# Optimization experiments

Hardware: AMD Instinct MI355X
Metric: run time of the kernel (lower is better)

## Reference

```python
import jax, jax.numpy as jnp
import numpy as np

EPS = 1e-8
LN_EPS = 1e-5
NEG = -1e9
H, E, D, P = 4, 32, 8, 64          # heads, embed_dim, head_dim, particles (= input_dim)
N_LAYERS, N_CLS = 4, 2
N_BATCH = 2048
F_EXTRA = 60                        # x feature channels; F_EXTRA + 4 == P == input_dim


def _ln(x):
    m = jnp.mean(x, -1, keepdims=True)
    v = jnp.mean((x - m) ** 2, -1, keepdims=True)
    return (x - m) * jax.lax.rsqrt(v + LN_EPS)


def _lin(x, w, b):
    return x @ w.T + b


def _gelu(x):
    return jax.nn.gelu(x, approximate=False)


def _mha(q_in, kv, in_w, in_b, out_w, out_b, attn_bias, kpm):
    # torch nn.MultiheadAttention, batch_first=False. q_in: (L,N,E), kv: (S,N,E)
    L, N, _ = q_in.shape
    S = kv.shape[0]
    q = _lin(q_in, in_w[:E], in_b[:E]) * (D ** -0.5)
    k = _lin(kv, in_w[E:2 * E], in_b[E:2 * E])
    v = _lin(kv, in_w[2 * E:], in_b[2 * E:])
    q = q.reshape(L, N, H, D); k = k.reshape(S, N, H, D); v = v.reshape(S, N, H, D)
    s = jnp.einsum('lnhd,snhd->nhls', q, k)
    if attn_bias is not None:
        s = s + attn_bias.reshape(N, H, L, S)
    s = jnp.where(kpm[:, None, None, :], NEG, s)
    a = jax.nn.softmax(s, -1)
    o = jnp.einsum('nhls,snhd->lnhd', a, v).reshape(L, N, E)
    return _lin(o, out_w, out_b)


def _jet_features(v):
    # vectorized calculate_jet_features_; v: (N,4,P). All pair features are symmetric,
    # diagonal stays zero (python loop skipped i==j), features are detached.
    e, px, py, pz = v[:, 0], v[:, 1], v[:, 2], v[:, 3]
    pt = jnp.sqrt(px ** 2 + py ** 2 + EPS)
    y = 0.5 * jnp.log((e + pz + EPS) / (e - pz + EPS))
    phi = jnp.mod(jnp.arctan2(py, px + EPS), 2.0 * np.pi)   # already in [0, 2pi)
    r = lambda a: a[:, :, None]
    c = lambda a: a[:, None, :]
    dist = (r(px) + c(px)) ** 2 + (r(py) + c(py)) ** 2 + (r(pz) + c(pz)) ** 2
    delta = jnp.sqrt(jnp.abs((r(y) - c(y)) ** 2 + (r(phi) - c(phi)) ** 2))
    pmin = jnp.minimum(r(pt), c(pt))
    kt = pmin * delta
    z = pmin / (r(pt) + c(pt) + EPS)
    m2 = r(e) ** 2 + c(e) ** 2 - dist
    f = jnp.stack([delta, kt, z, m2], axis=1)               # (N,4,P,P)
    f = f * (1.0 - jnp.eye(v.shape[2], dtype=f.dtype))
    return jax.lax.stop_gradient(f)


def _conv2d(x, w, b, stride, pad):
    y = jax.lax.conv_general_dilated(x, w, (stride, stride), [(pad, pad), (pad, pad)],
                                     dimension_numbers=('NCHW', 'OIHW', 'NCHW'))
    return y + b[None, :, None, None]


def _forward(x, four_momenta, jet_inputs, bn_w, bn_b, e1_w, e1_b, e2_w, e2_b,
             c1_w, c1_b, c2_w, c2_b,
             pb_in_w, pb_in_b, pb_out_w, pb_out_b, pb_f1_w, pb_f1_b, pb_f2_w, pb_f2_b, pb_wres,
             cb_in_w, cb_in_b, cb_out_w, cb_out_b, cb_f1_w, cb_f1_b, cb_f2_w, cb_f2_b, cb_wres,
             cb_cattn, cls_token, norm_w, norm_b, m1_w, m1_b, mh_w, mh_b, mf_w, mf_b):
    N = x.shape[0]
    xc = jnp.concatenate([x, four_momenta], axis=1)                 # (N, P, P): channels == particles
    kpm = ~(jnp.arange(P)[None, :] < jet_inputs[:, 1][:, None])     # (N, P) True = padded key
    xb = jnp.transpose(xc, (0, 2, 1))                               # (N, C=P, L=input_dim)
    mu = jnp.mean(xb, axis=(0, 2), keepdims=True)
    var = jnp.var(xb, axis=(0, 2), keepdims=True)
    xb = (xb - mu) * jax.lax.rsqrt(var + LN_EPS) * bn_w[None, :, None] + bn_b[None, :, None]
    h = jnp.transpose(xb, (2, 0, 1))                                # (seq, N, P)
    h = _gelu(_lin(_ln(h), e1_w, e1_b))
    h = _gelu(_lin(_ln(h), e2_w, e2_b))                             # (P, N, E)
    # --- PairEmbed: pairwise kinematic features -> 2 convs -> per-head attention bias
    f = _jet_features(four_momenta)                                 # (N, 4, P, P)
    cpe = _conv2d(f, c1_w, c1_b, 4, 0)                              # (N, H, 16, 16)
    cpe = _conv2d(cpe, c2_w, c2_b, 2, 1)                            # (N, H, 9, 9)
    bias = cpe.reshape(N * H, 9, 9)
    bias = jnp.pad(bias, ((0, 0), (0, P - 9), (0, P - 9)))          # additive bias zero-padded to (N*H,P,P)
    # --- particle blocks
    for i in range(N_LAYERS):
        res = h
        a = _ln(h)
        a = _mha(a, a, pb_in_w[i], pb_in_b[i], pb_out_w[i], pb_out_b[i], bias, kpm)
        h = _ln(a) + res
        res = h
        g = _gelu(_lin(_ln(h), pb_f1_w[i], pb_f1_b[i]))
        g = _lin(_ln(g), pb_f2_w[i], pb_f2_b[i])
        h = g + pb_wres[i] * res
    # --- class-attention blocks
    kpm_cls = jnp.concatenate([jnp.zeros((N, 1), dtype=bool), kpm], axis=1)
    cls = jnp.broadcast_to(cls_token, (1, N, E))
    for i in range(N_CLS):
        res = cls
        u = _ln(jnp.concatenate([cls, h], axis=0))                  # pre_attn_norm on keys/values only
        a = _mha(cls, u, cb_in_w[i], cb_in_b[i], cb_out_w[i], cb_out_b[i], None, kpm_cls)
        # tbhd,h->tbdh then reshape flattens as (d, h) order, matching torch
        a = jnp.einsum('tbhd,h->tbdh', a.reshape(1, N, H, D), cb_cattn[i]).reshape(1, N, E)
        cls = _ln(a) + res
        res = cls
        g = _gelu(_lin(_ln(cls), cb_f1_w[i], cb_f1_b[i]))
        g = _lin(_ln(g), cb_f2_w[i], cb_f2_b[i])
        cls = g + cb_wres[i] * res
    # --- head: affine LayerNorm + MLP (the two transposes in MLP cancel)
    z = (_ln(cls) * norm_w + norm_b)[0]                             # (N, E)
    z = jax.nn.relu(_lin(z, m1_w, m1_b))
    z = jax.nn.relu(_lin(z, mh_w, mh_b))
    z = jax.nn.sigmoid(_lin(z, mf_w, mf_b))                         # (N, 1)
    return z.reshape(-1)


def setup_inputs():
    key = jax.random.key(0)
    ks = jax.random.split(key, 40)
    w = lambda k, s: (0.05 * jax.random.normal(k, s)).astype(jnp.float32)
    p3 = jax.random.normal(ks[0], (N_BATCH, 3, P), dtype=jnp.float32)
    en = jnp.sqrt(jnp.sum(p3 ** 2, axis=1, keepdims=True) + 0.1)    # physical: E > |pz|
    four_momenta = jnp.concatenate([en, p3], axis=1)
    return {
        'x': jax.random.normal(ks[1], (N_BATCH, F_EXTRA, P), dtype=jnp.float32),
        'four_momenta': four_momenta,
        'jet_inputs': jax.random.randint(ks[2], (N_BATCH, 2), 1, P + 1),
        'bn_w': jnp.ones((P,), jnp.float32), 'bn_b': jnp.zeros((P,), jnp.float32),
        'e1_w': w(ks[3], (64, P)), 'e1_b': w(ks[4], (64,)),
        'e2_w': w(ks[5], (E, 64)), 'e2_b': w(ks[6], (E,)),
        'c1_w': w(ks[7], (H, 4, 4, 4)), 'c1_b': w(ks[8], (H,)),
        'c2_w': w(ks[9], (H, H, 2, 2)), 'c2_b': w(ks[10], (H,)),
        'pb_in_w': w(ks[11], (N_LAYERS, 3 * E, E)), 'pb_in_b': w(ks[12], (N_LAYERS, 3 * E)),
        'pb_out_w': w(ks[13], (N_LAYERS, E, E)), 'pb_out_b': w(ks[14], (N_LAYERS, E)),
        'pb_f1_w': w(ks[15], (N_LAYERS, 2 * E, E)), 'pb_f1_b': w(ks[16], (N_LAYERS, 2 * E)),
        'pb_f2_w': w(ks[17], (N_LAYERS, E, 2 * E)), 'pb_f2_b': w(ks[18], (N_LAYERS, E)),
        'pb_wres': jnp.ones((N_LAYERS, E), jnp.float32),
        'cb_in_w': w(ks[19], (N_CLS, 3 * E, E)), 'cb_in_b': w(ks[20], (N_CLS, 3 * E)),
        'cb_out_w': w(ks[21], (N_CLS, E, E)), 'cb_out_b': w(ks[22], (N_CLS, E)),
        'cb_f1_w': w(ks[23], (N_CLS, 2 * E, E)), 'cb_f1_b': w(ks[24], (N_CLS, 2 * E)),
        'cb_f2_w': w(ks[25], (N_CLS, E, 2 * E)), 'cb_f2_b': w(ks[26], (N_CLS, E)),
        'cb_wres': jnp.ones((N_CLS, E), jnp.float32),
        'cb_cattn': jnp.ones((N_CLS, H), jnp.float32),
        'cls_token': w(ks[27], (1, 1, E)),
        'norm_w': jnp.ones((E,), jnp.float32), 'norm_b': jnp.zeros((E,), jnp.float32),
        'm1_w': w(ks[28], (32, E)), 'm1_b': w(ks[29], (32,)),
        'mh_w': w(ks[30], (32, 32)), 'mh_b': w(ks[31], (32,)),
        'mf_w': w(ks[32], (1, 32)), 'mf_b': w(ks[33], (1,)),
    }


def reference(x, four_momenta, jet_inputs, bn_w, bn_b, e1_w, e1_b, e2_w, e2_b,
              c1_w, c1_b, c2_w, c2_b,
              pb_in_w, pb_in_b, pb_out_w, pb_out_b, pb_f1_w, pb_f1_b, pb_f2_w, pb_f2_b, pb_wres,
              cb_in_w, cb_in_b, cb_out_w, cb_out_b, cb_f1_w, cb_f1_b, cb_f2_w, cb_f2_b, cb_wres,
              cb_cattn, cls_token, norm_w, norm_b, m1_w, m1_b, mh_w, mh_b, mf_w, mf_b):
    return _forward(x, four_momenta, jet_inputs, bn_w, bn_b, e1_w, e1_b, e2_w, e2_b,
                    c1_w, c1_b, c2_w, c2_b,
                    pb_in_w, pb_in_b, pb_out_w, pb_out_b, pb_f1_w, pb_f1_b, pb_f2_w, pb_f2_b, pb_wres,
                    cb_in_w, cb_in_b, cb_out_w, cb_out_b, cb_f1_w, cb_f1_b, cb_f2_w, cb_f2_b, cb_wres,
                    cb_cattn, cls_token, norm_w, norm_b, m1_w, m1_b, mh_w, mh_b, mf_w, mf_b)
```

## Files before the change

kernel.cpp:

```cpp
#include <hip/hip_runtime.h>


__device__ __forceinline__ float4 ld4(const float* p){ return *reinterpret_cast<const float4*>(p); }
__device__ __forceinline__ float dot4(float4 a, float4 b){ return a.x*b.x + a.y*b.y + a.z*b.z + a.w*b.w; }
__device__ __forceinline__ float geluf(float v){ return 0.5f*v*(1.0f + erff(v*0.70710678118654752f)); }

__global__ void bn_stats_partial(const float* __restrict__ x, const float* __restrict__ fm,
                                 float* __restrict__ part) {
  int p  = threadIdx.x & 63;
  int rg = threadIdx.x >> 6;
  float s = 0.f, s2 = 0.f;
  for (int R = blockIdx.x*4 + rg; R < 2048*64; R += 1024) {
    int n_ = R >> 6, c = R & 63;
    float v = (c < 60) ? x[n_*3840 + c*64 + p] : fm[n_*256 + (c-60)*64 + p];
    s += v; s2 += v*v;
  }
  __shared__ float sm[256], sm2[256];
  sm[threadIdx.x] = s; sm2[threadIdx.x] = s2;
  __syncthreads();
  if (threadIdx.x < 64) {
    part[blockIdx.x*128 + p]      = sm[p]+sm[64+p]+sm[128+p]+sm[192+p];
    part[blockIdx.x*128 + 64 + p] = sm2[p]+sm2[64+p]+sm2[128+p]+sm2[192+p];
  }
}

__global__ void bn_stats_final(const float* __restrict__ part, float* __restrict__ stats) {
  int p = threadIdx.x;
  float s = 0.f, s2 = 0.f;
  for (int b = 0; b < 256; b++){ s += part[b*128+p]; s2 += part[b*128+64+p]; }
  float mean = s * (1.f/131072.f);
  float var  = s2 * (1.f/131072.f) - mean*mean;
  stats[p]      = mean;
  stats[64+p]   = rsqrtf(var + 1e-5f);
}

__device__ __forceinline__ void ln_rows32(const float* src, float* dst, int tid){
  int r = tid>>2, g = tid&3;
  const float* row = src + r*36;
  float v[8]; float s = 0.f;
  #pragma unroll
  for (int k=0;k<8;k++){ v[k] = row[g*8+k]; s += v[k]; }
  s += __shfl_xor(s,1); s += __shfl_xor(s,2);
  float mean = s * 0.03125f;
  float q = 0.f;
  #pragma unroll
  for (int k=0;k<8;k++){ float d = v[k]-mean; q += d*d; }
  q += __shfl_xor(q,1); q += __shfl_xor(q,2);
  float irs = rsqrtf(q*0.03125f + 1e-5f);
  float* drow = dst + r*36;
  #pragma unroll
  for (int k=0;k<8;k++) drow[g*8+k] = (v[k]-mean)*irs;
}

__device__ __forceinline__ void ln_rows64(const float* src, float* dst, int tid){
  int r = tid>>2, g = tid&3;
  const float* row = src + r*68;
  float v[16]; float s = 0.f;
  #pragma unroll
  for (int k=0;k<16;k++){ v[k] = row[g*16+k]; s += v[k]; }
  s += __shfl_xor(s,1); s += __shfl_xor(s,2);
  float mean = s * 0.015625f;
  float q = 0.f;
  #pragma unroll
  for (int k=0;k<16;k++){ float d = v[k]-mean; q += d*d; }
  q += __shfl_xor(q,1); q += __shfl_xor(q,2);
  float irs = rsqrtf(q*0.015625f + 1e-5f);
  float* drow = dst + r*68;
  #pragma unroll
  for (int k=0;k<16;k++) drow[g*16+k] = (v[k]-mean)*irs;
}

__global__ __launch_bounds__(256) void k_feat(
    const float* __restrict__ fm,
    const float* __restrict__ c1w_g, const float* __restrict__ c1b_g,
    const float* __restrict__ c2w_g, const float* __restrict__ c2b_g,
    float* __restrict__ G_bias)
{
  const int n   = blockIdx.x;
  const int tid = threadIdx.x;
  __shared__ float PQ[448];
  __shared__ float C1O[1024];
  __shared__ float CW[328];

  if (tid < 64) {
    int p = tid;
    float e_  = fm[n*256 + p];
    float px_ = fm[n*256 + 64 + p];
    float py_ = fm[n*256 + 128 + p];
    float pz_ = fm[n*256 + 192 + p];
    float pt_ = sqrtf(px_*px_ + py_*py_ + 1e-8f);
    float y_  = 0.5f * logf((e_ + pz_ + 1e-8f) / (e_ - pz_ + 1e-8f));
    float ph_ = atan2f(py_, px_ + 1e-8f);
    if (ph_ < 0.f) ph_ += 6.283185307179586f;
    PQ[0*64+p]=e_; PQ[1*64+p]=px_; PQ[2*64+p]=py_; PQ[3*64+p]=pz_;
    PQ[4*64+p]=pt_; PQ[5*64+p]=y_; PQ[6*64+p]=ph_;
  }
  CW[tid < 256 ? tid : 0] = c1w_g[tid < 256 ? tid : 0];
  if (tid < 4)  CW[256+tid] = c1b_g[tid];
  if (tid < 64) CW[260+tid] = c2w_g[tid];
  if (tid < 4)  CW[324+tid] = c2b_g[tid];
  __syncthreads();

  {
    int ho = tid>>4, wo = tid&15;
    float a0=0.f,a1=0.f,a2=0.f,a3=0.f;
    #pragma unroll 1
    for (int kh=0; kh<4; kh++){
      int r = ho*4+kh;
      float er=PQ[r], pxr=PQ[64+r], pyr=PQ[128+r], pzr=PQ[192+r], ptr_=PQ[256+r], yr=PQ[320+r], phr=PQ[384+r];
      #pragma unroll
      for (int kw=0; kw<4; kw++){
        int c = wo*4+kw;
        if (r == c) continue;
        float ec=PQ[c], pxc=PQ[64+c], pyc=PQ[128+c], pzc=PQ[192+c], ptc=PQ[256+c], yc=PQ[320+c], phc=PQ[384+c];
        float dy = yr-yc, dp = phr-phc;
        float delta = sqrtf(fabsf(dy*dy + dp*dp));
        float pmin = fminf(ptr_, ptc);
        float kt = pmin * delta;
        float zz = pmin / (ptr_ + ptc + 1e-8f);
        float sx_ = pxr+pxc, sy_ = pyr+pyc, sz_ = pzr+pzc;
        float m2 = er*er + ec*ec - (sx_*sx_ + sy_*sy_ + sz_*sz_);
        int wb = kh*4+kw;
// ... 78 lines not shown
      #pragma unroll
      for (int i=0;i<4;i++) acc[i][o] = b; }
    #pragma unroll 2
    for (int j=0;j<64;j+=4){
      float4 av[4], wv[4];
      #pragma unroll
      for (int i=0;i<4;i++) av[i] = ld4(SY + (tg*4+i)*68 + j);
      #pragma unroll
      for (int o=0;o<4;o++) wv[o] = ld4(SW + (og*4+o)*68 + j);
      #pragma unroll
      for (int i=0;i<4;i++)
        #pragma unroll
        for (int o=0;o<4;o++) acc[i][o] += dot4(av[i], wv[o]);
    }
    __syncthreads();
    #pragma unroll
    for (int i=0;i<4;i++)
      #pragma unroll
      for (int o=0;o<4;o++) SX[(tg*4+i)*68 + og*4+o] = geluf(acc[i][o]);
  }
  __syncthreads();

  ln_rows64(SX, SY, tid);
  for (int idx = tid; idx < 2048; idx += 256){ SW[(idx>>6)*68 + (idx&63)] = e2w[idx]; }
  for (int idx = tid; idx < 32; idx += 256) SW[4352+idx] = e2b[idx];
  __syncthreads();

  {
    int tg = tid>>4, og = tid&15;
    float acc[4][2];
    #pragma unroll
    for (int o=0;o<2;o++){ float b = SW[4352+og*2+o];
      #pragma unroll
      for (int i=0;i<4;i++) acc[i][o] = b; }
    #pragma unroll 2
    for (int j=0;j<64;j+=4){
      float4 av[4], wv[2];
      #pragma unroll
      for (int i=0;i<4;i++) av[i] = ld4(SY + (tg*4+i)*68 + j);
      #pragma unroll
      for (int o=0;o<2;o++) wv[o] = ld4(SW + (og*2+o)*68 + j);
      #pragma unroll
      for (int i=0;i<4;i++)
        #pragma unroll
        for (int o=0;o<2;o++) acc[i][o] += dot4(av[i], wv[o]);
    }
    #pragma unroll
    for (int i=0;i<4;i++)
      #pragma unroll
      for (int o=0;o<2;o++) G_h[n*2048 + (tg*4+i)*32 + og*2+o] = geluf(acc[i][o]);
  }
}

__global__ __launch_bounds__(256, 3) void k_layer(
    const int* __restrict__ ji,
    const float* __restrict__ in_w,  const float* __restrict__ in_b,
    const float* __restrict__ out_w, const float* __restrict__ out_b,
    const float* __restrict__ f1w,   const float* __restrict__ f1b,
    const float* __restrict__ f2w,   const float* __restrict__ f2b,
    const float* __restrict__ wres,
    float* __restrict__ G_h, const float* __restrict__ G_bias)
{
  const int n   = blockIdx.x;
  const int tid = threadIdx.x;

  __shared__ __align__(16) float SH[64*36];
  __shared__ __align__(16) float SX[64*36];
  __shared__ __align__(16) float SY[64*68];
  __shared__ __align__(16) float SW[3584];
  __shared__ float SBIAS[324];
  __shared__ int s_njet;

  if (tid == 0) s_njet = ji[n*2+1];
  for (int idx = tid; idx < 2048; idx += 256) {
    int t = idx>>5, e = idx&31;
    SH[t*36 + e] = G_h[n*2048 + idx];
  }
  for (int idx = tid; idx < 324; idx += 256) SBIAS[idx] = G_bias[n*324 + idx];
  __syncthreads();

  ln_rows32(SH, SX, tid);
  for (int idx = tid; idx < 3072; idx += 256){ SW[(idx>>5)*36 + (idx&31)] = in_w[idx]; }
  for (int idx = tid; idx < 96; idx += 256) SW[3456+idx] = in_b[idx];
  __syncthreads();

  {
    int tg = tid>>4, og = tid&15;
    float acc[4][4];
    #pragma unroll
    for (int o=0;o<4;o++){ float b = SW[3456+32+og*4+o];
      #pragma unroll
      for (int i=0;i<4;i++) acc[i][o] = b; }
    #pragma unroll 2
    for (int j=0;j<32;j+=4){
      float4 av[4], wv[4];
      #pragma unroll
      for (int i=0;i<4;i++) av[i] = ld4(SX + (tg*4+i)*36 + j);
      #pragma unroll
      for (int o=0;o<4;o++) wv[o] = ld4(SW + (32+og*4+o)*36 + j);
      #pragma unroll
      for (int i=0;i<4;i++)
        #pragma unroll
        for (int o=0;o<4;o++) acc[i][o] += dot4(av[i], wv[o]);
    }
    #pragma unroll
    for (int i=0;i<4;i++)
      #pragma unroll
      for (int o=0;o<4;o++){
        int ew = 32 + og*4+o, t = tg*4+i;
        if (ew < 64) SY[(ew-32)*68 + t] = acc[i][o];
        else         SY[2176 + (ew-64)*68 + t] = acc[i][o];
      }
  }
  __syncthreads();

  float od[8];
  {
    int hh = tid>>6, l = tid&63;
    float qd[8];
    #pragma unroll
    for (int d=0;d<8;d++){
      int e = hh*8+d;
      float a_ = SW[3456+e];
      #pragma unroll
      for (int k=0;k<8;k++) a_ += dot4(ld4(SX + l*36 + k*4), ld4(SW + e*36 + k*4));
      qd[d] = a_ * 0.35355339059327373f;
    }
    int njet = s_njet;
    float m = -3.4e38f, lsum = 0.f;
    #pragma unroll
    for (int d=0;d<8;d++) od[d] = 0.f;
    #pragma unroll 1
    for (int s0 = 0; s0 < 64; s0 += 16) {
      float sc[16];
      #pragma unroll
      for (int j=0;j<16;j++) sc[j]=0.f;
      #pragma unroll
      for (int d=0;d<8;d++){
        const float* kr = SY + (hh*8+d)*68 + s0;
        float qv = qd[d];
        #pragma unroll
        for (int j=0;j<16;j+=4){
          float4 kv4 = ld4(kr+j);
          sc[j]  +=qv*kv4.x; sc[j+1]+=qv*kv4.y;
          sc[j+2]+=qv*kv4.z; sc[j+3]+=qv*kv4.w;
        }
      }
      float cm = -3.4e38f;
      #pragma unroll
      for (int j=0;j<16;j++){
        int s = s0+j;
        float a_ = sc[j];
        if (s0 == 0 && l < 9 && j < 9) a_ += SBIAS[hh*81 + l*9 + j];
        a_ = (s >= njet) ? -1000000000.0f : a_;
        sc[j] = a_;
        cm = fmaxf(cm, a_);
      }
      float nm = fmaxf(m, cm);
      float corr = __expf(m - nm);
      lsum *= corr;
      #pragma unroll
      for (int d=0;d<8;d++) od[d] *= corr;
      #pragma unroll
      for (int j=0;j<16;j++){ sc[j] = __expf(sc[j]-nm); lsum += sc[j]; }
      #pragma unroll
      for (int d=0;d<8;d++){
        const float* vr = SY + 2176 + (hh*8+d)*68 + s0;
        float a_ = 0.f;
        #pragma unroll
        for (int j=0;j<16;j+=4){
          float4 vv = ld4(vr+j);
          a_ += sc[j]*vv.x + sc[j+1]*vv.y + sc[j+2]*vv.z + sc[j+3]*vv.w;
        }
        od[d] += a_;
      }
      m = nm;
    }
    float inv = 1.f/lsum;
    #pragma unroll
    for (int d=0;d<8;d++) od[d] *= inv;
  }
  __syncthreads();
  {
    int hh = tid>>6, l = tid&63;
    #pragma unroll
    for (int d=0;d<8;d++) SX[l*36 + hh*8 + d] = od[d];
  }
  for (int idx = tid; idx < 1024; idx += 256){ SW[(idx>>5)*36 + (idx&31)] = out_w[idx]; }
  for (int idx = tid; idx < 32; idx += 256) SW[3456+idx] = out_b[idx];
  __syncthreads();

  {
    int tg = tid>>4, og = tid&15;
    float acc[4][2];
    #pragma unroll
    for (int o=0;o<2;o++){ float b = SW[3456+og*2+o];
      #pragma unroll
      for (int i=0;i<4;i++) acc[i][o] = b; }
    #pragma unroll 2
    for (int j=0;j<32;j+=4){
      float4 av[4], wv[2];
      #pragma unroll
      for (int i=0;i<4;i++) av[i] = ld4(SX + (tg*4+i)*36 + j);
      #pragma unroll
      for (int o=0;o<2;o++) wv[o] = ld4(SW + (og*2+o)*36 + j);
      #pragma unroll
      for (int i=0;i<4;i++)
        #pragma unroll
        for (int o=0;o<2;o++) acc[i][o] += dot4(av[i], wv[o]);
    }
    #pragma unroll
    for (int i=0;i<4;i++)
      #pragma unroll
      for (int o=0;o<2;o++) SY[(tg*4+i)*36 + og*2+o] = acc[i][o];
  }
  __syncthreads();

  {
    int r = tid>>2, g = tid&3;
    const float* row = SY + r*36;
    float v[8]; float s = 0.f;
    #pragma unroll
    for (int k=0;k<8;k++){ v[k] = row[g*8+k]; s += v[k]; }
    s += __shfl_xor(s,1); s += __shfl_xor(s,2);
    float mean = s * 0.03125f;
    float q = 0.f;
    #pragma unroll
    for (int k=0;k<8;k++){ float d = v[k]-mean; q += d*d; }
    q += __shfl_xor(q,1); q += __shfl_xor(q,2);
    float irs = rsqrtf(q*0.03125f + 1e-5f);
    #pragma unroll
    for (int k=0;k<8;k++){ int e = g*8+k; SH[r*36+e] = (v[k]-mean)*irs + SH[r*36+e]; }
  }
  __syncthreads();

  ln_rows32(SH, SX, tid);
  for (int idx = tid; idx < 2048; idx += 256){ SW[(idx>>5)*36 + (idx&31)] = f1w[idx]; }
  for (int idx = tid; idx < 64; idx += 256) SW[3456+idx] = f1b[idx];
  __syncthreads();

  {
    int tg = tid>>4, og = tid&15;
    float acc[4][4];
    #pragma unroll
    for (int o=0;o<4;o++){ float b = SW[3456+og*4+o];
      #pragma unroll
      for (int i=0;i<4;i++) acc[i][o] = b; }
    #pragma unroll 2
    for (int j=0;j<32;j+=4){
      float4 av[4], wv[4];
      #pragma unroll
      for (int i=0;i<4;i++) av[i] = ld4(SX + (tg*4+i)*36 + j);
      #pragma unroll
      for (int o=0;o<4;o++) wv[o] = ld4(SW + (og*4+o)*36 + j);
      #pragma unroll
      for (int i=0;i<4;i++)
        #pragma unroll
        for (int o=0;o<4;o++) acc[i][o] += dot4(av[i], wv[o]);
    }
    #pragma unroll
    for (int i=0;i<4;i++)
      #pragma unroll
      for (int o=0;o<4;o++) SY[(tg*4+i)*68 + og*4+o] = geluf(acc[i][o]);
  }
  __syncthreads();

  {
    int r = tid>>2, g = tid&3;
    float* row = SY + r*68;
    float v[16]; float s = 0.f;
    #pragma unroll
    for (int k=0;k<16;k++){ v[k] = row[g*16+k]; s += v[k]; }
    s += __shfl_xor(s,1); s += __shfl_xor(s,2);
    float mean = s * 0.015625f;
    float q = 0.f;
    #pragma unroll
    for (int k=0;k<16;k++){ float d = v[k]-mean; q += d*d; }
    q += __shfl_xor(q,1); q += __shfl_xor(q,2);
    float irs = rsqrtf(q*0.015625f + 1e-5f);
    #pragma unroll
    for (int k=0;k<16;k++) row[g*16+k] = (v[k]-mean)*irs;
  }
  for (int idx = tid; idx < 2048; idx += 256){ SW[(idx>>6)*68 + (idx&63)] = f2w[idx]; }
  for (int idx = tid; idx < 32; idx += 256){ SW[3456+idx] = f2b[idx]; SW[3488+idx] = wres[idx]; }
  __syncthreads();

  {
    int tg = tid>>4, og = tid&15;
    float acc[4][2];
    #pragma unroll
    for (int o=0;o<2;o++){ float b = SW[3456+og*2+o];
      #pragma unroll
      for (int i=0;i<4;i++) acc[i][o] = b; }
    #pragma unroll 2
    for (int j=0;j<64;j+=4){
      float4 av[4], wv[2];
      #pragma unroll
      for (int i=0;i<4;i++) av[i] = ld4(SY + (tg*4+i)*68 + j);
      #pragma unroll
      for (int o=0;o<2;o++) wv[o] = ld4(SW + (og*2+o)*68 + j);
      #pragma unroll
      for (int i=0;i<4;i++)
        #pragma unroll
        for (int o=0;o<2;o++) acc[i][o] += dot4(av[i], wv[o]);
    }
    #pragma unroll
    for (int i=0;i<4;i++)
      #pragma unroll
      for (int o=0;o<2;o++){
        int e = og*2+o, t = tg*4+i;
        G_h[n*2048 + t*32 + e] = acc[i][o] + SW[3488+e]*SH[t*36+e];
      }
  }
}

__global__ __launch_bounds__(256, 3) void k_cls(
    const int* __restrict__ ji,
    const float* __restrict__ cb_in_w, const float* __restrict__ cb_in_b,
    const float* __restrict__ cb_out_w, const float* __restrict__ cb_out_b,
    const float* __restrict__ cb_f1_w, const float* __restrict__ cb_f1_b,
    const float* __restrict__ cb_f2_w, const float* __restrict__ cb_f2_b,
    const float* __restrict__ cb_wres, const float* __restrict__ cb_cattn,
    const float* __restrict__ cls_tok, const float* __restrict__ norm_w, const float* __restrict__ norm_b,
    const float* __restrict__ m1w, const float* __restrict__ m1b,
    const float* __restrict__ mhw, const float* __restrict__ mhb,
    const float* __restrict__ mfw, const float* __restrict__ mfb,
    const float* __restrict__ G_h, float* __restrict__ out)
{
  const int n   = blockIdx.x;
  const int tid = threadIdx.x;

  __shared__ __align__(16) float SX[64*36];
  __shared__ __align__(16) float SY[64*68];
  __shared__ __align__(16) float SW[3584];
  __shared__ __align__(16) float SV[320];
  __shared__ __align__(16) float csh[32];
  __shared__ int s_njet;

  if (tid == 0) s_njet = ji[n*2+1];
  for (int idx = tid; idx < 2048; idx += 256) {
    int t = idx>>5, e = idx&31;
    SX[t*36 + e] = G_h[n*2048 + idx];
  }
  __syncthreads();

  ln_rows32(SX, SX, tid);
  if (tid < 32) csh[tid] = cls_tok[tid];
  __syncthreads();

  for (int cl = 0; cl < 2; cl++) {
    const float* iw = cb_in_w + cl*3072;
    const float* ib = cb_in_b + cl*96;

    if (tid < 32) {
      float v = csh[tid];
      float s = v;
      s += __shfl_xor(s,1); s += __shfl_xor(s,2); s += __shfl_xor(s,4); s += __shfl_xor(s,8); s += __shfl_xor(s,16);
      float mean = s * 0.03125f;
      float d = v - mean;
      float q = d*d;
      q += __shfl_xor(q,1); q += __shfl_xor(q,2); q += __shfl_xor(q,4); q += __shfl_xor(q,8); q += __shfl_xor(q,16);
      float irs = rsqrtf(q*0.03125f + 1e-5f);
      SV[tid] = d*irs;
    }
    for (int idx = tid; idx < 3072; idx += 256){ SW[(idx>>5)*36 + (idx&31)] = iw[idx]; }
    for (int idx = tid; idx < 96; idx += 256) SW[3456+idx] = ib[idx];
    __syncthreads();

    if (tid < 32) {
      int e = tid;
      float a_ = SW[3456+e];
      #pragma unroll
      for (int k=0;k<8;k++) a_ += dot4(ld4(&csh[k*4]), ld4(SW + e*36 + k*4));
      SV[32+e] = a_ * 0.35355339059327373f;
    }
    if (tid < 64) {
      int ew = 32 + tid;
      float a_ = SW[3456+ew];
      #pragma unroll
      for (int k=0;k<8;k++) a_ += dot4(ld4(SV + k*4), ld4(SW + ew*36 + k*4));
      if (ew < 64) SY[(ew-32)*68] = a_;
      else         SY[2176 + (ew-64)*68] = a_;
    }
    {
      int tg = tid>>4, og = tid&15;
      float acc[4][4];
      #pragma unroll
      for (int o=0;o<4;o++){ float b = SW[3456+32+og*4+o];
        #pragma unroll
        for (int i=0;i<4;i++) acc[i][o] = b; }
      #pragma unroll 2
      for (int j=0;j<32;j+=4){
        float4 av[4], wv[4];
        #pragma unroll
        for (int i=0;i<4;i++) av[i] = ld4(SX + (tg*4+i)*36 + j);
        #pragma unroll
        for (int o=0;o<4;o++) wv[o] = ld4(SW + (32+og*4+o)*36 + j);
        #pragma unroll
        for (int i=0;i<4;i++)
          #pragma unroll
          for (int o=0;o<4;o++) acc[i][o] += dot4(av[i], wv[o]);
      }
// ... 146 lines not shown
                              hipStream_t stream) {
  (void)in_sizes; (void)n_in; (void)out_size; (void)ws_size;
  const float* x     = (const float*)d_in[0];
  const float* fm    = (const float*)d_in[1];
  const int*   ji    = (const int*)  d_in[2];
  const float* bn_w  = (const float*)d_in[3];
  const float* bn_b  = (const float*)d_in[4];
  const float* e1w   = (const float*)d_in[5];
  const float* e1b   = (const float*)d_in[6];
  const float* e2w   = (const float*)d_in[7];
  const float* e2b   = (const float*)d_in[8];
  const float* c1w   = (const float*)d_in[9];
  const float* c1b   = (const float*)d_in[10];
  const float* c2w   = (const float*)d_in[11];
  const float* c2b   = (const float*)d_in[12];
  const float* pb_in_w  = (const float*)d_in[13];
  const float* pb_in_b  = (const float*)d_in[14];
  const float* pb_out_w = (const float*)d_in[15];
  const float* pb_out_b = (const float*)d_in[16];
  const float* pb_f1_w  = (const float*)d_in[17];
  const float* pb_f1_b  = (const float*)d_in[18];
  const float* pb_f2_w  = (const float*)d_in[19];
  const float* pb_f2_b  = (const float*)d_in[20];
  const float* pb_wres  = (const float*)d_in[21];
  const float* cb_in_w  = (const float*)d_in[22];
  const float* cb_in_b  = (const float*)d_in[23];
  const float* cb_out_w = (const float*)d_in[24];
  const float* cb_out_b = (const float*)d_in[25];
  const float* cb_f1_w  = (const float*)d_in[26];
  const float* cb_f1_b  = (const float*)d_in[27];
  const float* cb_f2_w  = (const float*)d_in[28];
  const float* cb_f2_b  = (const float*)d_in[29];
  const float* cb_wres  = (const float*)d_in[30];
  const float* cb_cattn = (const float*)d_in[31];
  const float* cls_tok  = (const float*)d_in[32];
  const float* norm_w   = (const float*)d_in[33];
  const float* norm_b   = (const float*)d_in[34];
  const float* m1w      = (const float*)d_in[35];
  const float* m1b      = (const float*)d_in[36];
  const float* mhw      = (const float*)d_in[37];
  const float* mhb      = (const float*)d_in[38];
  const float* mfw      = (const float*)d_in[39];
  const float* mfb      = (const float*)d_in[40];

  float* part   = (float*)d_ws;
  float* stats  = part + 32768;
  float* G_h    = part + 40960;
  float* G_bias = G_h + 2048*2048;

  bn_stats_partial<<<256, 256, 0, stream>>>(x, fm, part);
  bn_stats_final<<<1, 64, 0, stream>>>(part, stats);
  k_feat<<<2048, 256, 0, stream>>>(fm, c1w, c1b, c2w, c2b, G_bias);
  k_embed2<<<2048, 256, 0, stream>>>(x, fm, stats, bn_w, bn_b, e1w, e1b, e2w, e2b, G_h);
  for (int li = 0; li < 4; li++) {
    k_layer<<<2048, 256, 0, stream>>>(ji,
        pb_in_w + li*3072, pb_in_b + li*96,
        pb_out_w + li*1024, pb_out_b + li*32,
        pb_f1_w + li*2048, pb_f1_b + li*64,
        pb_f2_w + li*2048, pb_f2_b + li*32,
        pb_wres + li*32, G_h, G_bias);
  }
  k_cls<<<2048, 256, 0, stream>>>(ji, cb_in_w, cb_in_b, cb_out_w, cb_out_b,
                                  cb_f1_w, cb_f1_b, cb_f2_w, cb_f2_b,
                                  cb_wres, cb_cattn, cls_tok, norm_w, norm_b,
                                  m1w, m1b, mhw, mhb, mfw, mfb, G_h, (float*)d_out);
}
```

Baseline: 585.9 us.

## Fuse four particle-attention layers and class head into one persistent kernel

Replaces four separate per-layer launches plus the class-token kernel with a single kernel that keeps each jet's hidden state in shared memory across all four layers and the class-attention stage. This removes the repeated global round-trips of the 2048x64x32 hidden tensor, the repeated bias loads and the extra launches. LayerNorm helpers and some shared stores are also vectorised with float4. Shared memory per block grows (SH, SBIAS and SV all live together), which may lower occupancy below the requested three blocks per CU.

```diff
diff --git a/kernel.cpp b/kernel.cpp
--- a/kernel.cpp
+++ b/kernel.cpp
@@ -2,6 +2,7 @@
 
 
 __device__ __forceinline__ float4 ld4(const float* p){ return *reinterpret_cast<const float4*>(p); }
+__device__ __forceinline__ void st4(float* p, float4 v){ *reinterpret_cast<float4*>(p) = v; }
 __device__ __forceinline__ float dot4(float4 a, float4 b){ return a.x*b.x + a.y*b.y + a.z*b.z + a.w*b.w; }
 __device__ __forceinline__ float geluf(float v){ return 0.5f*v*(1.0f + erff(v*0.70710678118654752f)); }
 
@@ -36,38 +37,41 @@
 
 __device__ __forceinline__ void ln_rows32(const float* src, float* dst, int tid){
   int r = tid>>2, g = tid&3;
-  const float* row = src + r*36;
-  float v[8]; float s = 0.f;
-  #pragma unroll
-  for (int k=0;k<8;k++){ v[k] = row[g*8+k]; s += v[k]; }
+  const float* row = src + r*36 + g*8;
+  float4 a = ld4(row), b = ld4(row+4);
+  float s = a.x+a.y+a.z+a.w + b.x+b.y+b.z+b.w;
   s += __shfl_xor(s,1); s += __shfl_xor(s,2);
   float mean = s * 0.03125f;
-  float q = 0.f;
-  #pragma unroll
-  for (int k=0;k<8;k++){ float d = v[k]-mean; q += d*d; }
+  float4 da = make_float4(a.x-mean,a.y-mean,a.z-mean,a.w-mean);
+  float4 db = make_float4(b.x-mean,b.y-mean,b.z-mean,b.w-mean);
+  float q = dot4(da,da) + dot4(db,db);
   q += __shfl_xor(q,1); q += __shfl_xor(q,2);
   float irs = rsqrtf(q*0.03125f + 1e-5f);
-  float* drow = dst + r*36;
-  #pragma unroll
-  for (int k=0;k<8;k++) drow[g*8+k] = (v[k]-mean)*irs;
+  float* drow = dst + r*36 + g*8;
+  st4(drow,   make_float4(da.x*irs, da.y*irs, da.z*irs, da.w*irs));
+  st4(drow+4, make_float4(db.x*irs, db.y*irs, db.z*irs, db.w*irs));
 }
 
 __device__ __forceinline__ void ln_rows64(const float* src, float* dst, int tid){
   int r = tid>>2, g = tid&3;
-  const float* row = src + r*68;
-  float v[16]; float s = 0.f;
-  #pragma unroll
-  for (int k=0;k<16;k++){ v[k] = row[g*16+k]; s += v[k]; }
+  const float* row = src + r*68 + g*16;
+  float4 v0 = ld4(row), v1 = ld4(row+4), v2 = ld4(row+8), v3 = ld4(row+12);
+  float s = v0.x+v0.y+v0.z+v0.w + v1.x+v1.y+v1.z+v1.w
+          + v2.x+v2.y+v2.z+v2.w + v3.x+v3.y+v3.z+v3.w;
   s += __shfl_xor(s,1); s += __shfl_xor(s,2);
   float mean = s * 0.015625f;
-  float q = 0.f;
-  #pragma unroll
-  for (int k=0;k<16;k++){ float d = v[k]-mean; q += d*d; }
+  float4 d0 = make_float4(v0.x-mean,v0.y-mean,v0.z-mean,v0.w-mean);
+  float4 d1 = make_float4(v1.x-mean,v1.y-mean,v1.z-mean,v1.w-mean);
+  float4 d2 = make_float4(v2.x-mean,v2.y-mean,v2.z-mean,v2.w-mean);
+  float4 d3 = make_float4(v3.x-mean,v3.y-mean,v3.z-mean,v3.w-mean);
+  float q = dot4(d0,d0)+dot4(d1,d1)+dot4(d2,d2)+dot4(d3,d3);
   q += __shfl_xor(q,1); q += __shfl_xor(q,2);
   float irs = rsqrtf(q*0.015625f + 1e-5f);
-  float* drow = dst + r*68;
-  #pragma unroll
-  for (int k=0;k<16;k++) drow[g*16+k] = (v[k]-mean)*irs;
+  float* drow = dst + r*68 + g*16;
+  st4(drow,    make_float4(d0.x*irs,d0.y*irs,d0.z*irs,d0.w*irs));
+  st4(drow+4,  make_float4(d1.x*irs,d1.y*irs,d1.z*irs,d1.w*irs));
+  st4(drow+8,  make_float4(d2.x*irs,d2.y*irs,d2.z*irs,d2.w*irs));
+  st4(drow+12, make_float4(d3.x*irs,d3.y*irs,d3.z*irs,d3.w*irs));
 }
 
 __global__ __launch_bounds__(256) void k_feat(
@@ -252,270 +256,13 @@
   }
 }
 
-__global__ __launch_bounds__(256, 3) void k_layer(
+__global__ __launch_bounds__(256, 3) void k_tail(
     const int* __restrict__ ji,
-    const float* __restrict__ in_w,  const float* __restrict__ in_b,
-    const float* __restrict__ out_w, const float* __restrict__ out_b,
-    const float* __restrict__ f1w,   const float* __restrict__ f1b,
-    const float* __restrict__ f2w,   const float* __restrict__ f2b,
-    const float* __restrict__ wres,
-    float* __restrict__ G_h, const float* __restrict__ G_bias)
-{
-  const int n   = blockIdx.x;
-  const int tid = threadIdx.x;
-
-  __shared__ __align__(16) float SH[64*36];
-  __shared__ __align__(16) float SX[64*36];
-  __shared__ __align__(16) float SY[64*68];
-  __shared__ __align__(16) float SW[3584];
-  __shared__ float SBIAS[324];
-  __shared__ int s_njet;
-
-  if (tid == 0) s_njet = ji[n*2+1];
-  for (int idx = tid; idx < 2048; idx += 256) {
-    int t = idx>>5, e = idx&31;
-    SH[t*36 + e] = G_h[n*2048 + idx];
-  }
-  for (int idx = tid; idx < 324; idx += 256) SBIAS[idx] = G_bias[n*324 + idx];
-  __syncthreads();
-
-  ln_rows32(SH, SX, tid);
-  for (int idx = tid; idx < 3072; idx += 256){ SW[(idx>>5)*36 + (idx&31)] = in_w[idx]; }
-  for (int idx = tid; idx < 96; idx += 256) SW[3456+idx] = in_b[idx];
-  __syncthreads();
-
-  {
-    int tg = tid>>4, og = tid&15;
-    float acc[4][4];
-    #pragma unroll
-    for (int o=0;o<4;o++){ float b = SW[3456+32+og*4+o];
-      #pragma unroll
-      for (int i=0;i<4;i++) acc[i][o] = b; }
-    #pragma unroll 2
-    for (int j=0;j<32;j+=4){
-      float4 av[4], wv[4];
-      #pragma unroll
-      for (int i=0;i<4;i++) av[i] = ld4(SX + (tg*4+i)*36 + j);
-      #pragma unroll
-      for (int o=0;o<4;o++) wv[o] = ld4(SW + (32+og*4+o)*36 + j);
-      #pragma unroll
-      for (int i=0;i<4;i++)
-        #pragma unroll
-        for (int o=0;o<4;o++) acc[i][o] += dot4(av[i], wv[o]);
-    }
-    #pragma unroll
-    for (int i=0;i<4;i++)
-      #pragma unroll
-      for (int o=0;o<4;o++){
-        int ew = 32 + og*4+o, t = tg*4+i;
-        if (ew < 64) SY[(ew-32)*68 + t] = acc[i][o];
-        else         SY[2176 + (ew-64)*68 + t] = acc[i][o];
-      }
-  }
-  __syncthreads();
-
-  float od[8];
-  {
-    int hh = tid>>6, l = tid&63;
-    float qd[8];
-    #pragma unroll
-    for (int d=0;d<8;d++){
-      int e = hh*8+d;
-      float a_ = SW[3456+e];
-      #pragma unroll
-      for (int k=0;k<8;k++) a_ += dot4(ld4(SX + l*36 + k*4), ld4(SW + e*36 + k*4));
-      qd[d] = a_ * 0.35355339059327373f;
-    }
-    int njet = s_njet;
-    float m = -3.4e38f, lsum = 0.f;
-    #pragma unroll
-    for (int d=0;d<8;d++) od[d] = 0.f;
-    #pragma unroll 1
-    for (int s0 = 0; s0 < 64; s0 += 16) {
-      float sc[16];
-      #pragma unroll
-      for (int j=0;j<16;j++) sc[j]=0.f;
-      #pragma unroll
-      for (int d=0;d<8;d++){
-        const float* kr = SY + (hh*8+d)*68 + s0;
-        float qv = qd[d];
-        #pragma unroll
-        for (int j=0;j<16;j+=4){
-          float4 kv4 = ld4(kr+j);
-          sc[j]  +=qv*kv4.x; sc[j+1]+=qv*kv4.y;
-          sc[j+2]+=qv*kv4.z; sc[j+3]+=qv*kv4.w;
-        }
-      }
-      float cm = -3.4e38f;
-      #pragma unroll
-      for (int j=0;j<16;j++){
-        int s = s0+j;
-        float a_ = sc[j];
-        if (s0 == 0 && l < 9 && j < 9) a_ += SBIAS[hh*81 + l*9 + j];
-        a_ = (s >= njet) ? -1000000000.0f : a_;
-        sc[j] = a_;
-        cm = fmaxf(cm, a_);
-      }
-      float nm = fmaxf(m, cm);
-      float corr = __expf(m - nm);
-      lsum *= corr;
-      #pragma unroll
-      for (int d=0;d<8;d++) od[d] *= corr;
-      #pragma unroll
-      for (int j=0;j<16;j++){ sc[j] = __expf(sc[j]-nm); lsum += sc[j]; }
-      #pragma unroll
-      for (int d=0;d<8;d++){
-        const float* vr = SY + 2176 + (hh*8+d)*68 + s0;
-        float a_ = 0.f;
-        #pragma unroll
-        for (int j=0;j<16;j+=4){
-          float4 vv = ld4(vr+j);
-          a_ += sc[j]*vv.x + sc[j+1]*vv.y + sc[j+2]*vv.z + sc[j+3]*vv.w;
-        }
-        od[d] += a_;
-      }
-      m = nm;
-    }
-    float inv = 1.f/lsum;
-    #pragma unroll
-    for (int d=0;d<8;d++) od[d] *= inv;
-  }
-  __syncthreads();
-  {
-    int hh = tid>>6, l = tid&63;
-    #pragma unroll
-    for (int d=0;d<8;d++) SX[l*36 + hh*8 + d] = od[d];
-  }
-  for (int idx = tid; idx < 1024; idx += 256){ SW[(idx>>5)*36 + (idx&31)] = out_w[idx]; }
-  for (int idx = tid; idx < 32; idx += 256) SW[3456+idx] = out_b[idx];
-  __syncthreads();
-
-  {
-    int tg = tid>>4, og = tid&15;
-    float acc[4][2];
-    #pragma unroll
-    for (int o=0;o<2;o++){ float b = SW[3456+og*2+o];
-      #pragma unroll
-      for (int i=0;i<4;i++) acc[i][o] = b; }
-    #pragma unroll 2
-    for (int j=0;j<32;j+=4){
-      float4 av[4], wv[2];
-      #pragma unroll
-      for (int i=0;i<4;i++) av[i] = ld4(SX + (tg*4+i)*36 + j);
-      #pragma unroll
-      for (int o=0;o<2;o++) wv[o] = ld4(SW + (og*2+o)*36 + j);
-      #pragma unroll
-      for (int i=0;i<4;i++)
-        #pragma unroll
-        for (int o=0;o<2;o++) acc[i][o] += dot4(av[i], wv[o]);
-    }
-    #pragma unroll
-    for (int i=0;i<4;i++)
-      #pragma unroll
-      for (int o=0;o<2;o++) SY[(tg*4+i)*36 + og*2+o] = acc[i][o];
-  }
-  __syncthreads();
-
-  {
-    int r = tid>>2, g = tid&3;
-    const float* row = SY + r*36;
-    float v[8]; float s = 0.f;
-    #pragma unroll
-    for (int k=0;k<8;k++){ v[k] = row[g*8+k]; s += v[k]; }
-    s += __shfl_xor(s,1); s += __shfl_xor(s,2);
-    float mean = s * 0.03125f;
-    float q = 0.f;
-    #pragma unroll
-    for (int k=0;k<8;k++){ float d = v[k]-mean; q += d*d; }
-    q += __shfl_xor(q,1); q += __shfl_xor(q,2);
-    float irs = rsqrtf(q*0.03125f + 1e-5f);
-    #pragma unroll
-    for (int k=0;k<8;k++){ int e = g*8+k; SH[r*36+e] = (v[k]-mean)*irs + SH[r*36+e]; }
-  }
-  __syncthreads();
-
-  ln_rows32(SH, SX, tid);
-  for (int idx = tid; idx < 2048; idx += 256){ SW[(idx>>5)*36 + (idx&31)] = f1w[idx]; }
-  for (int idx = tid; idx < 64; idx += 256) SW[3456+idx] = f1b[idx];
-  __syncthreads();
-
-  {
-    int tg = tid>>4, og = tid&15;
-    float acc[4][4];
-    #pragma unroll
-    for (int o=0;o<4;o++){ float b = SW[3456+og*4+o];
-      #pragma unroll
-      for (int i=0;i<4;i++) acc[i][o] = b; }
-    #pragma unroll 2
-    for (int j=0;j<32;j+=4){
-      float4 av[4], wv[4];
-      #pragma unroll
-      for (int i=0;i<4;i++) av[i] = ld4(SX + (tg*4+i)*36 + j);
-      #pragma unroll
-      for (int o=0;o<4;o++) wv[o] = ld4(SW + (og*4+o)*36 + j);
-      #pragma unroll
-      for (int i=0;i<4;i++)
-        #pragma unroll
-        for (int o=0;o<4;o++) acc[i][o] += dot4(av[i], wv[o]);
-    }
-    #pragma unroll
-    for (int i=0;i<4;i++)
-      #pragma unroll
-      for (int o=0;o<4;o++) SY[(tg*4+i)*68 + og*4+o] = geluf(acc[i][o]);
-  }
-  __syncthreads();
-
-  {
-    int r = tid>>2, g = tid&3;
-    float* row = SY + r*68;
-    float v[16]; float s = 0.f;
-    #pragma unroll
-    for (int k=0;k<16;k++){ v[k] = row[g*16+k]; s += v[k]; }
-    s += __shfl_xor(s,1); s += __shfl_xor(s,2);
-    float mean = s * 0.015625f;
-    float q = 0.f;
-    #pragma unroll
-    for (int k=0;k<16;k++){ float d = v[k]-mean; q += d*d; }
-    q += __shfl_xor(q,1); q += __shfl_xor(q,2);
-    float irs = rsqrtf(q*0.015625f + 1e-5f);
-    #pragma unroll
-    for (int k=0;k<16;k++) row[g*16+k] = (v[k]-mean)*irs;
-  }
-  for (int idx = tid; idx < 2048; idx += 256){ SW[(idx>>6)*68 + (idx&63)] = f2w[idx]; }
-  for (int idx = tid; idx < 32; idx += 256){ SW[3456+idx] = f2b[idx]; SW[3488+idx] = wres[idx]; }
-  __syncthreads();
-
-  {
-    int tg = tid>>4, og = tid&15;
-    float acc[4][2];
-    #pragma unroll
-    for (int o=0;o<2;o++){ float b = SW[3456+og*2+o];
-      #pragma unroll
-      for (int i=0;i<4;i++) acc[i][o] = b; }
-    #pragma unroll 2
-    for (int j=0;j<64;j+=4){
-      float4 av[4], wv[2];
-      #pragma unroll
-      for (int i=0;i<4;i++) av[i] = ld4(SY + (tg*4+i)*68 + j);
-      #pragma unroll
-      for (int o=0;o<2;o++) wv[o] = ld4(SW + (og*2+o)*68 + j);
-      #pragma unroll
-      for (int i=0;i<4;i++)
-        #pragma unroll
-        for (int o=0;o<2;o++) acc[i][o] += dot4(av[i], wv[o]);
-    }
-    #pragma unroll
-    for (int i=0;i<4;i++)
-      #pragma unroll
-      for (int o=0;o<2;o++){
-        int e = og*2+o, t = tg*4+i;
-        G_h[n*2048 + t*32 + e] = acc[i][o] + SW[3488+e]*SH[t*36+e];
-      }
-  }
-}
-
-__global__ __launch_bounds__(256, 3) void k_cls(
-    const int* __restrict__ ji,
+    const float* __restrict__ pb_in_w,  const float* __restrict__ pb_in_b,
+    const float* __restrict__ pb_out_w, const float* __restrict__ pb_out_b,
+    const float* __restrict__ pb_f1_w,  const float* __restrict__ pb_f1_b,
+    const float* __restrict__ pb_f2_w,  const float* __restrict__ pb_f2_b,
+    const float* __restrict__ pb_wres,
     const float* __restrict__ cb_in_w, const float* __restrict__ cb_in_b,
     const float* __restrict__ cb_out_w, const float* __restrict__ cb_out_b,
     const float* __restrict__ cb_f1_w, const float* __restrict__ cb_f1_b,
@@ -525,29 +272,288 @@
     const float* __restrict__ m1w, const float* __restrict__ m1b,
     const float* __restrict__ mhw, const float* __restrict__ mhb,
     const float* __restrict__ mfw, const float* __restrict__ mfb,
-    const float* __restrict__ G_h, float* __restrict__ out)
+    const float* __restrict__ G_h, const float* __restrict__ G_bias,
+    float* __restrict__ out)
 {
   const int n   = blockIdx.x;
   const int tid = threadIdx.x;
 
+  __shared__ __align__(16) float SH[64*36];
   __shared__ __align__(16) float SX[64*36];
   __shared__ __align__(16) float SY[64*68];
   __shared__ __align__(16) float SW[3584];
+  __shared__ float SBIAS[324];
   __shared__ __align__(16) float SV[320];
   __shared__ __align__(16) float csh[32];
   __shared__ int s_njet;
 
   if (tid == 0) s_njet = ji[n*2+1];
-  for (int idx = tid; idx < 2048; idx += 256) {
-    int t = idx>>5, e = idx&31;
-    SX[t*36 + e] = G_h[n*2048 + idx];
-  }
-  __syncthreads();
-
-  ln_rows32(SX, SX, tid);
+  for (int idx = tid; idx < 512; idx += 256) {
+    float4 v = ld4(G_h + n*2048 + idx*4);
+    int t = idx>>3, e = (idx&7)*4;
+    st4(&SH[t*36 + e], v);
+  }
+  for (int idx = tid; idx < 324; idx += 256) SBIAS[idx] = G_bias[n*324 + idx];
+  __syncthreads();
+
+  #pragma unroll 1
+  for (int li = 0; li < 4; li++) {
+    const float* in_w  = pb_in_w  + li*3072;
+    const float* in_b  = pb_in_b  + li*96;
+    const float* out_w = pb_out_w + li*1024;
+    const float* out_b = pb_out_b + li*32;
+    const float* f1w   = pb_f1_w  + li*2048;
+    const float* f1b   = pb_f1_b  + li*64;
+    const float* f2w   = pb_f2_w  + li*2048;
+    const float* f2b   = pb_f2_b  + li*32;
+    const float* wres  = pb_wres  + li*32;
+
+    ln_rows32(SH, SX, tid);
+    for (int idx = tid; idx < 3072; idx += 256){ SW[(idx>>5)*36 + (idx&31)] = in_w[idx]; }
+    for (int idx = tid; idx < 96; idx += 256) SW[3456+idx] = in_b[idx];
+    __syncthreads();
+
+    {
+      int tg = tid>>4, og = tid&15;
+      float acc[4][4];
+      #pragma unroll
+      for (int o=0;o<4;o++){ float b = SW[3456+32+og*4+o];
+        #pragma unroll
+        for (int i=0;i<4;i++) acc[i][o] = b; }
+      #pragma unroll 2
+      for (int j=0;j<32;j+=4){
+        float4 av[4], wv[4];
+        #pragma unroll
+        for (int i=0;i<4;i++) av[i] = ld4(SX + (tg*4+i)*36 + j);
+        #pragma unroll
+        for (int o=0;o<4;o++) wv[o] = ld4(SW + (32+og*4+o)*36 + j);
+        #pragma unroll
+        for (int i=0;i<4;i++)
+          #pragma unroll
+          for (int o=0;o<4;o++) acc[i][o] += dot4(av[i], wv[o]);
+      }
+      #pragma unroll
+      for (int i=0;i<4;i++)
+        #pragma unroll
+        for (int o=0;o<4;o++){
+          int ew = 32 + og*4+o, t = tg*4+i;
+          if (ew < 64) SY[(ew-32)*68 + t] = acc[i][o];
+          else         SY[2176 + (ew-64)*68 + t] = acc[i][o];
+        }
+    }
+    __syncthreads();
+
+    float od[8];
+    {
+      int hh = tid>>6, l = tid&63;
+      float qd[8];
+      #pragma unroll
+      for (int d=0;d<8;d++){
+        int e = hh*8+d;
+        float a_ = SW[3456+e];
+        #pragma unroll
+        for (int k=0;k<8;k++) a_ += dot4(ld4(SX + l*36 + k*4), ld4(SW + e*36 + k*4));
+        qd[d] = a_ * 0.35355339059327373f;
+      }
+      int njet = s_njet;
+      float m = -3.4e38f, lsum = 0.f;
+      #pragma unroll
+      for (int d=0;d<8;d++) od[d] = 0.f;
+      #pragma unroll 1
+      for (int s0 = 0; s0 < 64; s0 += 16) {
+        float sc[16];
+        #pragma unroll
+        for (int j=0;j<16;j++) sc[j]=0.f;
+        #pragma unroll
+        for (int d=0;d<8;d++){
+          const float* kr = SY + (hh*8+d)*68 + s0;
+          float qv = qd[d];
+          #pragma unroll
+          for (int j=0;j<16;j+=4){
+            float4 kv4 = ld4(kr+j);
+            sc[j]  +=qv*kv4.x; sc[j+1]+=qv*kv4.y;
+            sc[j+2]+=qv*kv4.z; sc[j+3]+=qv*kv4.w;
+          }
+        }
+        float cm = -3.4e38f;
+        #pragma unroll
+        for (int j=0;j<16;j++){
+          int s = s0+j;
+          float a_ = sc[j];
+          if (s0 == 0 && l < 9 && j < 9) a_ += SBIAS[hh*81 + l*9 + j];
+          a_ = (s >= njet) ? -1000000000.0f : a_;
+          sc[j] = a_;
+          cm = fmaxf(cm, a_);
+        }
+        float nm = fmaxf(m, cm);
+        float corr = __expf(m - nm);
+        lsum *= corr;
+        #pragma unroll
+        for (int d=0;d<8;d++) od[d] *= corr;
+        #pragma unroll
+        for (int j=0;j<16;j++){ sc[j] = __expf(sc[j]-nm); lsum += sc[j]; }
+        #pragma unroll
+        for (int d=0;d<8;d++){
+          const float* vr = SY + 2176 + (hh*8+d)*68 + s0;
+          float a_ = 0.f;
+          #pragma unroll
+          for (int j=0;j<16;j+=4){
+            float4 vv = ld4(vr+j);
+            a_ += sc[j]*vv.x + sc[j+1]*vv.y + sc[j+2]*vv.z + sc[j+3]*vv.w;
+          }
+          od[d] += a_;
+        }
+        m = nm;
+      }
+      float inv = 1.f/lsum;
+      #pragma unroll
+      for (int d=0;d<8;d++) od[d] *= inv;
+    }
+    __syncthreads();
+    {
+      int hh = tid>>6, l = tid&63;
+      st4(&SX[l*36 + hh*8],     make_float4(od[0],od[1],od[2],od[3]));
+      st4(&SX[l*36 + hh*8 + 4], make_float4(od[4],od[5],od[6],od[7]));
+    }
+    for (int idx = tid; idx < 1024; idx += 256){ SW[(idx>>5)*36 + (idx&31)] = out_w[idx]; }
+    for (int idx = tid; idx < 32; idx += 256) SW[3456+idx] = out_b[idx];
+    __syncthreads();
+
+    {
+      int tg = tid>>4, og = tid&15;
+      float acc[4][2];
+      #pragma unroll
+      for (int o=0;o<2;o++){ float b = SW[3456+og*2+o];
+        #pragma unroll
+        for (int i=0;i<4;i++) acc[i][o] = b; }
+      #pragma unroll 2
+      for (int j=0;j<32;j+=4){
+        float4 av[4], wv[2];
+        #pragma unroll
+        for (int i=0;i<4;i++) av[i] = ld4(SX + (tg*4+i)*36 + j);
+        #pragma unroll
+        for (int o=0;o<2;o++) wv[o] = ld4(SW + (og*2+o)*36 + j);
+        #pragma unroll
+        for (int i=0;i<4;i++)
+          #pragma unroll
+          for (int o=0;o<2;o++) acc[i][o] += dot4(av[i], wv[o]);
+      }
+      #pragma unroll
+      for (int i=0;i<4;i++)
+        #pragma unroll
+        for (int o=0;o<2;o++) SY[(tg*4+i)*36 + og*2+o] = acc[i][o];
+    }
+    __syncthreads();
+
+    {
+      int r = tid>>2, g = tid&3;
+      const float* row = SY + r*36 + g*8;
+      float4 a = ld4(row), b = ld4(row+4);
+      float s = a.x+a.y+a.z+a.w + b.x+b.y+b.z+b.w;
+      s += __shfl_xor(s,1); s += __shfl_xor(s,2);
+      float mean = s * 0.03125f;
+      float4 da = make_float4(a.x-mean,a.y-mean,a.z-mean,a.w-mean);
+      float4 db = make_float4(b.x-mean,b.y-mean,b.z-mean,b.w-mean);
+      float q = dot4(da,da) + dot4(db,db);
+      q += __shfl_xor(q,1); q += __shfl_xor(q,2);
+      float irs = rsqrtf(q*0.03125f + 1e-5f);
+      float* hrow = SH + r*36 + g*8;
+      float4 ha = ld4(hrow), hb = ld4(hrow+4);
+      st4(hrow,   make_float4(da.x*irs+ha.x, da.y*irs+ha.y, da.z*irs+ha.z, da.w*irs+ha.w));
+      st4(hrow+4, make_float4(db.x*irs+hb.x, db.y*irs+hb.y, db.z*irs+hb.z, db.w*irs+hb.w));
+    }
+    __syncthreads();
+
+    ln_rows32(SH, SX, tid);
+    for (int idx = tid; idx < 2048; idx += 256){ SW[(idx>>5)*36 + (idx&31)] = f1w[idx]; }
+    for (int idx = tid; idx < 64; idx += 256) SW[3456+idx] = f1b[idx];
+    __syncthreads();
+
+    {
+      int tg = tid>>4, og = tid&15;
+      float acc[4][4];
+      #pragma unroll
+      for (int o=0;o<4;o++){ float b = SW[3456+og*4+o];
+        #pragma unroll
+        for (int i=0;i<4;i++) acc[i][o] = b; }
+      #pragma unroll 2
+      for (int j=0;j<32;j+=4){
+        float4 av[4], wv[4];
+        #pragma unroll
+        for (int i=0;i<4;i++) av[i] = ld4(SX + (tg*4+i)*36 + j);
+        #pragma unroll
+        for (int o=0;o<4;o++) wv[o] = ld4(SW + (og*4+o)*36 + j);
+        #pragma unroll
+        for (int i=0;i<4;i++)
+          #pragma unroll
+          for (int o=0;o<4;o++) acc[i][o] += dot4(av[i], wv[o]);
+      }
+      #pragma unroll
+      for (int i=0;i<4;i++)
+        #pragma unroll
+        for (int o=0;o<4;o++) SY[(tg*4+i)*68 + og*4+o] = geluf(acc[i][o]);
+    }
+    __syncthreads();
+
+    {
+      int r = tid>>2, g = tid&3;
+      float* row = SY + r*68 + g*16;
+      float4 v0 = ld4(row), v1 = ld4(row+4), v2 = ld4(row+8), v3 = ld4(row+12);
+      float s = v0.x+v0.y+v0.z+v0.w + v1.x+v1.y+v1.z+v1.w
+              + v2.x+v2.y+v2.z+v2.w + v3.x+v3.y+v3.z+v3.w;
+      s += __shfl_xor(s,1); s += __shfl_xor(s,2);
+      float mean = s * 0.015625f;
+      float4 d0 = make_float4(v0.x-mean,v0.y-mean,v0.z-mean,v0.w-mean);
+      float4 d1 = make_float4(v1.x-mean,v1.y-mean,v1.z-mean,v1.w-mean);
+      float4 d2 = make_float4(v2.x-mean,v2.y-mean,v2.z-mean,v2.w-mean);
+      float4 d3 = make_float4(v3.x-mean,v3.y-mean,v3.z-mean,v3.w-mean);
+      float q = dot4(d0,d0)+dot4(d1,d1)+dot4(d2,d2)+dot4(d3,d3);
+      q += __shfl_xor(q,1); q += __shfl_xor(q,2);
+      float irs = rsqrtf(q*0.015625f + 1e-5f);
+      st4(row,    make_float4(d0.x*irs,d0.y*irs,d0.z*irs,d0.w*irs));
+      st4(row+4,  make_float4(d1.x*irs,d1.y*irs,d1.z*irs,d1.w*irs));
+      st4(row+8,  make_float4(d2.x*irs,d2.y*irs,d2.z*irs,d2.w*irs));
+      st4(row+12, make_float4(d3.x*irs,d3.y*irs,d3.z*irs,d3.w*irs));
+    }
+    for (int idx = tid; idx < 2048; idx += 256){ SW[(idx>>6)*68 + (idx&63)] = f2w[idx]; }
+    for (int idx = tid; idx < 32; idx += 256){ SW[3456+idx] = f2b[idx]; SW[3488+idx] = wres[idx]; }
+    __syncthreads();
+
+    {
+      int tg = tid>>4, og = tid&15;
+      float acc[4][2];
+      #pragma unroll
+      for (int o=0;o<2;o++){ float b = SW[3456+og*2+o];
+        #pragma unroll
+        for (int i=0;i<4;i++) acc[i][o] = b; }
+      #pragma unroll 2
+      for (int j=0;j<64;j+=4){
+        float4 av[4], wv[2];
+        #pragma unroll
+        for (int i=0;i<4;i++) av[i] = ld4(SY + (tg*4+i)*68 + j);
+        #pragma unroll
+        for (int o=0;o<2;o++) wv[o] = ld4(SW + (og*2+o)*68 + j);
+        #pragma unroll
+        for (int i=0;i<4;i++)
+          #pragma unroll
+          for (int o=0;o<2;o++) acc[i][o] += dot4(av[i], wv[o]);
+      }
+      #pragma unroll
+      for (int i=0;i<4;i++)
+        #pragma unroll
+        for (int o=0;o<2;o++){
+          int e = og*2+o, t = tg*4+i;
+          SH[t*36+e] = acc[i][o] + SW[3488+e]*SH[t*36+e];
+        }
+    }
+    __syncthreads();
+  }
+
+  ln_rows32(SH, SX, tid);
   if (tid < 32) csh[tid] = cls_tok[tid];
   __syncthreads();
 
+  #pragma unroll 1
   for (int cl = 0; cl < 2; cl++) {
     const float* iw = cb_in_w + cl*3072;
     const float* ib = cb_in_b + cl*96;
@@ -800,16 +806,9 @@
   bn_stats_final<<<1, 64, 0, stream>>>(part, stats);
   k_feat<<<2048, 256, 0, stream>>>(fm, c1w, c1b, c2w, c2b, G_bias);
   k_embed2<<<2048, 256, 0, stream>>>(x, fm, stats, bn_w, bn_b, e1w, e1b, e2w, e2b, G_h);
-  for (int li = 0; li < 4; li++) {
-    k_layer<<<2048, 256, 0, stream>>>(ji,
-        pb_in_w + li*3072, pb_in_b + li*96,
-        pb_out_w + li*1024, pb_out_b + li*32,
-        pb_f1_w + li*2048, pb_f1_b + li*64,
-        pb_f2_w + li*2048, pb_f2_b + li*32,
-        pb_wres + li*32, G_h, G_bias);
-  }
-  k_cls<<<2048, 256, 0, stream>>>(ji, cb_in_w, cb_in_b, cb_out_w, cb_out_b,
-                                  cb_f1_w, cb_f1_b, cb_f2_w, cb_f2_b,
-                                  cb_wres, cb_cattn, cls_tok, norm_w, norm_b,
-                                  m1w, m1b, mhw, mhb, mfw, mfb, G_h, (float*)d_out);
+  k_tail<<<2048, 256, 0, stream>>>(ji,
+      pb_in_w, pb_in_b, pb_out_w, pb_out_b, pb_f1_w, pb_f1_b, pb_f2_w, pb_f2_b, pb_wres,
+      cb_in_w, cb_in_b, cb_out_w, cb_out_b, cb_f1_w, cb_f1_b, cb_f2_w, cb_f2_b,
+      cb_wres, cb_cattn, cls_tok, norm_w, norm_b, m1w, m1b, mhw, mhb, mfw, mfb,
+      G_h, G_bias, (float*)d_out);
 }
```

Result: slower. 664.7 us (+13.4%).
